# Optimization experiments

Hardware: AMD Instinct MI355X
Metric: run time of the kernel (lower is better)

Reference implementation:

```python
import jax, jax.numpy as jnp
import numpy as np

SEQ, BS, IN, H, NUM_LAYERS = 512, 64, 1024, 1024, 2


def setup_inputs() -> dict:
    key = jax.random.key(0)
    k1, k2, k3, k4 = jax.random.split(key, 4)

    def xavier(k, shape):
        fan_in, fan_out = shape
        lim = jnp.sqrt(6.0 / (fan_in + fan_out))
        return jax.random.uniform(k, shape, jnp.float32, -lim, lim)

    return {
        "x": jax.random.normal(k1, (SEQ, BS, IN), jnp.float32),
        "W_ii0": xavier(k2, (IN, 4 * H)),
        "W_ii": xavier(k3, (H, 4 * H)),
        "W_hi": xavier(k4, (H, 4 * H)),
        "bias": jnp.zeros((4 * H,), jnp.float32),
    }


def _run_layer(x, W_in, W_hi, bias, hidden):
    # x: [seq, bs, feat]; precompute input projection for all timesteps at once
    xw = jnp.einsum('sbf,fg->sbg', x, W_in) + bias  # [seq, bs, 4H]
    bs = x.shape[1]

    def step(carry, xw_t):
        h, c = carry
        gates = xw_t + h @ W_hi  # [bs, 4H]
        i_t = jax.nn.sigmoid(gates[:, :hidden])
        f_t = jax.nn.sigmoid(gates[:, hidden:2 * hidden])
        g_t = jnp.tanh(gates[:, 2 * hidden:3 * hidden])
        o_t = jax.nn.sigmoid(gates[:, 3 * hidden:])
        c = f_t * c + i_t * g_t
        h = o_t * jnp.tanh(c)
        return (h, c), h

    h0 = jnp.zeros((bs, hidden), x.dtype)
    c0 = jnp.zeros((bs, hidden), x.dtype)
    (h, c), hs = jax.lax.scan(step, (h0, c0), xw)
    return hs, h, c  # hs: [seq, bs, hidden]


def reference(x, W_ii0, W_ii, W_hi, bias):
    h = c = None
    for l in range(NUM_LAYERS):
        W_in = W_ii0 if l == 0 else W_ii
        x, h, c = _run_layer(x, W_in, W_hi, bias, H)
    return x, (h, c)
```

## Files before the change

### kernel.cpp

```cpp
#include <hip/hip_runtime.h>

typedef __attribute__((ext_vector_type(8))) short short8;
typedef __attribute__((ext_vector_type(4))) float floatx4;

#define SEQ 512
#define BS  64
#define HID 1024
#define G4  4096
#define NBLK 128
#define NGRP 4
#define BPG  32
#define GBS  16
#define UPB  32

__device__ __forceinline__ unsigned short f2b(float f) {
  union { float f; unsigned u; } v; v.f = f;
  return (unsigned short)((v.u + 0x7FFFu + ((v.u >> 16) & 1u)) >> 16);
}
__device__ __forceinline__ float b2f(unsigned short s) {
  union { unsigned u; float f; } v; v.u = ((unsigned)s) << 16;
  return v.f;
}

__device__ __forceinline__ void gload_lds16_cc(const void* g, void* l) {
  __builtin_amdgcn_global_load_lds(
      (const __attribute__((address_space(1))) unsigned int*)g,
      (__attribute__((address_space(3))) unsigned int*)l,
      16, 0, 17);
}

__global__ void wtrans(const float* __restrict__ W, short* __restrict__ WT) {
  __shared__ float tile[32][33];
  const int tx = threadIdx.x, ty = threadIdx.y;
  const int n0 = blockIdx.x << 5, k0 = blockIdx.y << 5;
#pragma unroll
  for (int i = 0; i < 32; i += 8)
    tile[ty + i][tx] = W[(size_t)(k0 + ty + i) * G4 + n0 + tx];
  __syncthreads();
#pragma unroll
  for (int i = 0; i < 32; i += 8)
    WT[(size_t)(n0 + ty + i) * 1024 + k0 + tx] = (short)f2b(tile[tx][ty + i]);
}

__global__ __launch_bounds__(256)
void conv_bf16(const float* __restrict__ in, unsigned short* __restrict__ out) {
  const size_t i = ((size_t)blockIdx.x * 256 + threadIdx.x) * 8;
  const floatx4 a = *(const floatx4*)(in + i);
  const floatx4 b = *(const floatx4*)(in + i + 4);
  short8 s;
#pragma unroll
  for (int e = 0; e < 4; ++e) { s[e] = (short)f2b(a[e]); s[4 + e] = (short)f2b(b[e]); }
  *(short8*)(out + i) = s;
}

struct FusedArgs {
  const unsigned short* xw;
  const short* wt_hi;
  unsigned short* hbuf;
  float* cbuf;
  unsigned int* cnt;
  float* hs;
  unsigned short* hsb;
  float* h_final;
  float* c_final;
  int t0, t1, wr_final;
  const short* A;
  const short* BT;
  const float* bias;
  unsigned short* dst;
  int Mrows, genable;
};

__device__ __forceinline__ void scan_body(const FusedArgs& p, char* smem) {
  const int tid = threadIdx.x;
  const int wave = tid >> 6, lane = tid & 63;
  const int lr = lane & 15, lh = lane >> 4;
  const int blk = blockIdx.x;
  const int g = blk >> 5;
  const int ub_idx = blk & 31;
  const int u_new = (wave << 2) + (lr >> 2);
  const int gcol = ((lr & 3) << 10) + ub_idx * UPB + u_new;

  short8 breg[32];
  {
    const short* wp = p.wt_hi + (size_t)gcol * HID + (lh << 3);
#pragma unroll
    for (int kk = 0; kk < 32; ++kk) breg[kk] = *(const short8*)(wp + (kk << 5));
  }

  const int b_new = (lh << 2) + (lr & 3);
  const int ci = ((g * GBS + b_new) << 10) + ub_idx * UPB + u_new;
  float creg = p.cbuf[ci];
  const int asw = lr & 7;
  const int j0 = lr & 1, j1 = (lr >> 1) & 1;

  for (int t = p.t0; t < p.t1; ++t) {
    float xv[4];
#pragma unroll
    for (int r = 0; r < 4; ++r) {
      const size_t rowi = (size_t)(t - p.t0) * BS + g * GBS + (lh << 2) + r;
      xv[r] = b2f(p.xw[rowi * G4 + gcol]);
    }

    if (t > 0 && wave == 0) {
      const unsigned long long cad =
          (unsigned long long)(p.cnt + ((size_t)t * NGRP + g) * 16);
      unsigned f0;
      for (;;) {
        asm volatile("global_load_dword %0, %1, off sc0 sc1\n\t"
                     "s_waitcnt vmcnt(0)"
                     : "=v"(f0) : "v"(cad) : "memory");
        if (f0 >= BPG) break;
        __builtin_amdgcn_s_sleep(1);
      }
    }
    __syncthreads();

    const unsigned short* hb = p.hbuf + (size_t)(t & 1) * (BS * HID) + (size_t)g * GBS * HID;
    unsigned short* hw = p.hbuf + (size_t)((t + 1) & 1) * (BS * HID) + (size_t)g * GBS * HID;

    {
      const int spans[4] = { 2 * wave, 2 * wave + 16, 2 * wave + 1, 2 * wave + 17 };
#pragma unroll
      for (int j = 0; j < 4; ++j) {
        const int i = spans[j];
        const int row = i >> 1, half = i & 1;
        const int chunk = ((half << 6) + lane) ^ (row & 7);
        gload_lds16_cc(hb + row * HID + (chunk << 3), smem + (i << 10));
      }
    }
    asm volatile("s_waitcnt vmcnt(2)" ::: "memory");
    __builtin_amdgcn_s_barrier();
    __builtin_amdgcn_sched_barrier(0);

    floatx4 acc = {0.f, 0.f, 0.f, 0.f};
#pragma unroll
    for (int kk = 0; kk < 16; ++kk) {
      const int kc = (kk << 2) + lh;
      const short8 afr = *(const short8*)(smem + (lr << 11) + ((kc ^ asw) << 4));
      acc = __builtin_amdgcn_mfma_f32_16x16x32_bf16(afr, breg[kk], acc, 0, 0, 0);
    }
    asm volatile("s_waitcnt vmcnt(0)" ::: "memory");
    __builtin_amdgcn_s_barrier();
    __builtin_amdgcn_sched_barrier(0);
#pragma unroll
    for (int kk = 16; kk < 32; ++kk) {
      const int kc = (kk << 2) + lh;
      const short8 afr = *(const short8*)(smem + (lr << 11) + ((kc ^ asw) << 4));
      acc = __builtin_amdgcn_mfma_f32_16x16x32_bf16(afr, breg[kk], acc, 0, 0, 0);
    }

    const float x0 = acc[0] + xv[0], x1 = acc[1] + xv[1];
    const float x2 = acc[2] + xv[2], x3 = acc[3] + xv[3];
    const float s0 = __shfl_xor(x1, 1), s1 = __shfl_xor(x0, 1);
    const float s2 = __shfl_xor(x3, 1), s3 = __shfl_xor(x2, 1);
    const float y0 = j0 ? s0 : x0, y1 = j0 ? x1 : s1;
    const float y2 = j0 ? s2 : x2, y3 = j0 ? x3 : s3;
    const float z0s = __shfl_xor(y2, 2), z1s = __shfl_xor(y3, 2);
    const float z2s = __shfl_xor(y0, 2), z3s = __shfl_xor(y1, 2);
    const float ig = j1 ? z0s : y0;
    const float fg = j1 ? z1s : y1;
    const float gg = j1 ? y2 : z2s;
    const float og = j1 ? y3 : z3s;

    const float iv = 1.f / (1.f + __expf(-ig));
    const float fv = 1.f / (1.f + __expf(-fg));
    const float gv = tanhf(gg);
    const float ov = 1.f / (1.f + __expf(-og));
    const float cn = fv * creg + iv * gv;
    creg = cn;
    const float hv = ov * tanhf(cn);
    const unsigned hv16 = (unsigned)f2b(hv);

    {
      const unsigned other = (unsigned)__shfl_xor((int)hv16, 4, 64);
      if ((lr & 4) == 0) {
        const unsigned val = (hv16 & 0xFFFFu) | (other << 16);
        const unsigned long long dst =
            (unsigned long long)(hw + (size_t)b_new * HID + ub_idx * UPB + u_new);
        asm volatile("global_store_dword %0, %1, off sc0 sc1"
                     :: "v"(dst), "v"(val) : "memory");
      }
    }
    asm volatile("s_waitcnt vmcnt(0)" ::: "memory");
    __syncthreads();
    if (tid == 0)
      atomicAdd(p.cnt + ((size_t)(t + 1) * NGRP + g) * 16, 1u);

    {
      const size_t oidx = ((size_t)t * BS + g * GBS + b_new) * HID + ub_idx * UPB + u_new;
      p.hs[oidx] = hv;
      p.hsb[oidx] = (unsigned short)hv16;
      if (p.wr_final && t == SEQ - 1) { p.h_final[ci] = hv; p.c_final[ci] = cn; }
    }
  }
  p.cbuf[ci] = creg;
}

__device__ __forceinline__ void gemm_body(const FusedArgs& p, char* smem,
                                          int bi, int gstride) {
  if (!p.genable) return;
  short* Al = (short*)smem;
  short* Bl = (short*)(smem + 10240);
  const int tid = threadIdx.x;
  const int wave = tid >> 6, lane = tid & 63;
  const int lr = lane & 15, lh = lane >> 4;
  const int wm = wave >> 1, wn = wave & 1;
  const int nmt = p.Mrows >> 7;
  const int tot = nmt << 5;
  const int srow = tid >> 2, scol = (tid & 3) << 3;

  for (int tt = bi; tt < tot; tt += gstride) {
    const int m0 = (tt >> 5) << 7, n0 = (tt & 31) << 7;
    const short* aptr = p.A + (size_t)(m0 + srow) * 1024 + scol;
    const short* bptr = p.BT + (size_t)(n0 + srow) * 1024 + scol;
    floatx4 acc[2][4] = {};
    short8 pa = *(const short8*)aptr;
    short8 pb = *(const short8*)bptr;
    for (int it = 0; it < 32; ++it) {
      __syncthreads();
      *(short8*)&Al[srow * 40 + scol] = pa;
      *(short8*)&Bl[srow * 40 + scol] = pb;
      __syncthreads();
      if (it < 31) {
        pa = *(const short8*)(aptr + ((it + 1) << 5));
        pb = *(const short8*)(bptr + ((it + 1) << 5));
      }
      short8 af[2], bf[4];
#pragma unroll
      for (int mt = 0; mt < 2; ++mt)
        af[mt] = *(const short8*)&Al[(wm * 32 + mt * 16 + lr) * 40 + lh * 8];
#pragma unroll
      for (int nt = 0; nt < 4; ++nt)
        bf[nt] = *(const short8*)&Bl[(wn * 64 + nt * 16 + lr) * 40 + lh * 8];
#pragma unroll
      for (int mt = 0; mt < 2; ++mt)
#pragma unroll
        for (int nt = 0; nt < 4; ++nt)
          acc[mt][nt] = __builtin_amdgcn_mfma_f32_16x16x32_bf16(af[mt], bf[nt], acc[mt][nt], 0, 0, 0);
    }
#pragma unroll
    for (int nt = 0; nt < 4; ++nt) {
      const int gc = n0 + wn * 64 + nt * 16 + lr;
      const float bv = p.bias[gc];
#pragma unroll
      for (int mt = 0; mt < 2; ++mt)
#pragma unroll
        for (int r = 0; r < 4; ++r) {
          const int gr = m0 + wm * 32 + mt * 16 + (lh << 2) + r;
          p.dst[(size_t)gr * G4 + gc] = f2b(acc[mt][nt][r] + bv);
        }
    }
  }
}

__global__ __launch_bounds__(512, 2)
void gemm_pre(FusedArgs p) {
  __shared__ __align__(16) char smem[84480];
  gemm_body(p, smem, blockIdx.x, 2 * NBLK);
}

__global__ __launch_bounds__(512, 2)
void lstm_fused(FusedArgs p) {
  __shared__ __align__(16) char smem[84480];
  if (blockIdx.x < NBLK) scan_body(p, smem);
  else                   gemm_body(p, smem, blockIdx.x - NBLK, NBLK);
}

extern "C" void kernel_launch(void* const* d_in, const int* in_sizes, int n_in,
                              void* d_out, int out_size, void* d_ws, size_t ws_size,
                              hipStream_t stream) {
  const float* x    = (const float*)d_in[0];
  const float* Wii0 = (const float*)d_in[1];
  const float* Wii  = (const float*)d_in[2];
  const float* Whi  = (const float*)d_in[3];
  const float* bias = (const float*)d_in[4];
  float* out  = (float*)d_out;
  float* hs   = out;
  float* hfin = out + (size_t)SEQ * BS * HID;
  float* cfin = hfin + BS * HID;

  char* ws = (char*)d_ws;
  short* WT0 = (short*)ws;
  short* WT1 = WT0 + (size_t)G4 * 1024;
  short* WTh = WT1 + (size_t)G4 * 1024;
  unsigned short* hbuf = (unsigned short*)(WTh + (size_t)G4 * 1024);
  float* cbuf = (float*)(hbuf + 2 * BS * HID);
  unsigned int* cnt = (unsigned int*)(cbuf + BS * HID);
  unsigned short* xb = (unsigned short*)(cnt + (size_t)(SEQ + 1) * NGRP * 16);
  char* tail = (char*)(xb + (size_t)SEQ * BS * HID);
  const size_t head = (size_t)(tail - ws);
  const size_t avail = (ws_size > head) ? ws_size - head : 0;
  const size_t perT = (size_t)BS * G4 * 2;

  int chunk;
  if      (avail >= 2 * 128 * perT) chunk = 128;
  else if (avail >= 2 * 64  * perT) chunk = 64;
  else if (avail >= 2 * 32  * perT) chunk = 32;
  else                              chunk = 8;
  const size_t chunkBytes = (size_t)chunk * perT;
  unsigned short* xwbuf[2] = { (unsigned short*)tail,
                               (unsigned short*)(tail + chunkBytes) };
  const int nc = SEQ / chunk;

  wtrans<<<dim3(128, 32), dim3(32, 8), 0, stream>>>(Wii0, WT0);
  wtrans<<<dim3(128, 32), dim3(32, 8), 0, stream>>>(Wii, WT1);
  wtrans<<<dim3(128, 32), dim3(32, 8), 0, stream>>>(Whi, WTh);
  conv_bf16<<<dim3((SEQ * BS * HID) / (256 * 8)), dim3(256), 0, stream>>>(x, xb);

  for (int layer = 0; layer < 2; ++layer) {
    hipMemsetAsync(hbuf, 0, 2 * BS * HID * sizeof(unsigned short), stream);
    hipMemsetAsync(cbuf, 0, BS * HID * sizeof(float), stream);
    hipMemsetAsync(cnt, 0, (size_t)(SEQ + 1) * NGRP * 16 * sizeof(unsigned), stream);

    if (layer == 0) {
      FusedArgs pa = {};
      pa.A = (const short*)xb;
      pa.BT = WT0;
      pa.bias = bias;
      pa.dst = xwbuf[0];
      pa.Mrows = chunk * BS;
      pa.genable = 1;
      gemm_pre<<<dim3(2 * NBLK), dim3(512), 0, stream>>>(pa);
    }

    for (int c = 0; c < nc; ++c) {
      FusedArgs fa;
      fa.xw = xwbuf[c & 1];
      fa.wt_hi = WTh;
      fa.hbuf = hbuf;
      fa.cbuf = cbuf;
      fa.cnt = cnt;
      fa.hs = hs;
      fa.hsb = xb;
      fa.h_final = layer ? hfin : nullptr;
      fa.c_final = layer ? cfin : nullptr;
      fa.t0 = c * chunk;
      fa.t1 = (c + 1) * chunk;
      fa.wr_final = layer;
      fa.bias = bias;
      fa.dst = xwbuf[(c + 1) & 1];
      fa.Mrows = chunk * BS;
      const int nxt = ((c + 1) % nc) * chunk * BS;
      fa.A = (const short*)(xb + (size_t)nxt * HID);
      fa.BT = (layer == 0 && c < nc - 1) ? WT0 : WT1;
      fa.genable = !(layer == 1 && c == nc - 1);
      void* args[] = { &fa };
      hipLaunchCooperativeKernel(reinterpret_cast<const void*>(&lstm_fused),
                                 dim3(2 * NBLK), dim3(512), args, 0u, stream);
    }
  }
}
```

Measured before the change: 4.473 ms.

## Replace per-step atomic counter with per-block flags and stage h outputs through LDS

Cross-block step synchronization moves from one atomic counter per group and step to one flag per block holding the completed timestep. Waiters poll 32 flags in parallel across a wave and wait until all of them reach the step. The hidden-state results are also staged in LDS so that the h exchange buffer, the bf16 copy and the fp32 output are written with wide coalesced stores by separate waves, instead of scattered per-lane stores. The cost is an extra __syncthreads per step, and only wave 0's exchange store plus its flag store sits on the critical path before the next step's wait.

```diff
diff --git a/kernel.cpp b/kernel.cpp
--- a/kernel.cpp
+++ b/kernel.cpp
@@ -58,7 +58,7 @@
   const short* wt_hi;
   unsigned short* hbuf;
   float* cbuf;
-  unsigned int* cnt;
+  unsigned int* flags;
   float* hs;
   unsigned short* hsb;
   float* h_final;
@@ -72,6 +72,8 @@
 };
 
 __device__ __forceinline__ void scan_body(const FusedArgs& p, char* smem) {
+  unsigned short* hpk = (unsigned short*)(smem + 32768);
+  float* hpf = (float*)(smem + 34048);
   const int tid = threadIdx.x;
   const int wave = tid >> 6, lane = tid & 63;
   const int lr = lane & 15, lh = lane >> 4;
@@ -94,6 +96,9 @@
   const int asw = lr & 7;
   const int j0 = lr & 1, j1 = (lr >> 1) & 1;
 
+  const unsigned long long fad =
+      (unsigned long long)(p.flags + ((size_t)(g * BPG) + (lane & 31)) * 16);
+
   for (int t = p.t0; t < p.t1; ++t) {
     float xv[4];
 #pragma unroll
@@ -103,14 +108,12 @@
     }
 
     if (t > 0 && wave == 0) {
-      const unsigned long long cad =
-          (unsigned long long)(p.cnt + ((size_t)t * NGRP + g) * 16);
       unsigned f0;
       for (;;) {
         asm volatile("global_load_dword %0, %1, off sc0 sc1\n\t"
                      "s_waitcnt vmcnt(0)"
-                     : "=v"(f0) : "v"(cad) : "memory");
-        if (f0 >= BPG) break;
+                     : "=v"(f0) : "v"(fad) : "memory");
+        if (__all(f0 >= (unsigned)t)) break;
         __builtin_amdgcn_s_sleep(1);
       }
     }
@@ -170,28 +173,38 @@
     const float cn = fv * creg + iv * gv;
     creg = cn;
     const float hv = ov * tanhf(cn);
-    const unsigned hv16 = (unsigned)f2b(hv);
-
-    {
-      const unsigned other = (unsigned)__shfl_xor((int)hv16, 4, 64);
-      if ((lr & 4) == 0) {
-        const unsigned val = (hv16 & 0xFFFFu) | (other << 16);
-        const unsigned long long dst =
-            (unsigned long long)(hw + (size_t)b_new * HID + ub_idx * UPB + u_new);
+    const unsigned short hv16 = f2b(hv);
+
+    hpk[b_new * 40 + u_new] = hv16;
+    hpf[b_new * 36 + u_new] = hv;
+    if (p.wr_final && t == SEQ - 1) { p.h_final[ci] = hv; p.c_final[ci] = cn; }
+    __syncthreads();
+
+    if (wave == 0) {
+      const int row = lane >> 2, k = lane & 3;
+      const short8 v = *(const short8*)(smem + 32768 + row * 80 + k * 16);
+      const unsigned long long dst = (unsigned long long)
+          (hw + (size_t)row * HID + ub_idx * UPB + (k << 3));
+      asm volatile("global_store_dwordx4 %0, %1, off sc0 sc1"
+                   :: "v"(dst), "v"(v) : "memory");
+      asm volatile("s_waitcnt vmcnt(0)" ::: "memory");
+      if (lane == 0) {
+        const unsigned long long fdst =
+            (unsigned long long)(p.flags + (size_t)blk * 16);
+        const unsigned fval = (unsigned)(t + 1);
         asm volatile("global_store_dword %0, %1, off sc0 sc1"
-                     :: "v"(dst), "v"(val) : "memory");
+                     :: "v"(fdst), "v"(fval) : "memory");
       }
-    }
-    asm volatile("s_waitcnt vmcnt(0)" ::: "memory");
-    __syncthreads();
-    if (tid == 0)
-      atomicAdd(p.cnt + ((size_t)(t + 1) * NGRP + g) * 16, 1u);
-
-    {
-      const size_t oidx = ((size_t)t * BS + g * GBS + b_new) * HID + ub_idx * UPB + u_new;
-      p.hs[oidx] = hv;
-      p.hsb[oidx] = (unsigned short)hv16;
-      if (p.wr_final && t == SEQ - 1) { p.h_final[ci] = hv; p.c_final[ci] = cn; }
+    } else if (wave == 1) {
+      const int row = lane >> 2, k = lane & 3;
+      const short8 v = *(const short8*)(smem + 32768 + row * 80 + k * 16);
+      *(short8*)(p.hsb + ((size_t)t * BS + g * GBS + row) * HID
+                 + ub_idx * UPB + (k << 3)) = v;
+    } else if (wave < 4) {
+      const int row = ((wave - 2) << 3) + (lane >> 3), k = lane & 7;
+      const floatx4 v = *(const floatx4*)(smem + 34048 + row * 144 + k * 16);
+      *(floatx4*)(p.hs + ((size_t)t * BS + g * GBS + row) * HID
+                  + ub_idx * UPB + (k << 2)) = v;
     }
   }
   p.cbuf[ci] = creg;
@@ -286,8 +299,8 @@
   short* WTh = WT1 + (size_t)G4 * 1024;
   unsigned short* hbuf = (unsigned short*)(WTh + (size_t)G4 * 1024);
   float* cbuf = (float*)(hbuf + 2 * BS * HID);
-  unsigned int* cnt = (unsigned int*)(cbuf + BS * HID);
-  unsigned short* xb = (unsigned short*)(cnt + (size_t)(SEQ + 1) * NGRP * 16);
+  unsigned int* flags = (unsigned int*)(cbuf + BS * HID);
+  unsigned short* xb = (unsigned short*)(flags + NBLK * 16);
   char* tail = (char*)(xb + (size_t)SEQ * BS * HID);
   const size_t head = (size_t)(tail - ws);
   const size_t avail = (ws_size > head) ? ws_size - head : 0;
@@ -311,7 +324,7 @@
   for (int layer = 0; layer < 2; ++layer) {
     hipMemsetAsync(hbuf, 0, 2 * BS * HID * sizeof(unsigned short), stream);
     hipMemsetAsync(cbuf, 0, BS * HID * sizeof(float), stream);
-    hipMemsetAsync(cnt, 0, (size_t)(SEQ + 1) * NGRP * 16 * sizeof(unsigned), stream);
+    hipMemsetAsync(flags, 0, NBLK * 16 * sizeof(unsigned int), stream);
 
     if (layer == 0) {
       FusedArgs pa = {};
@@ -330,7 +343,7 @@
       fa.wt_hi = WTh;
       fa.hbuf = hbuf;
       fa.cbuf = cbuf;
-      fa.cnt = cnt;
+      fa.flags = flags;
       fa.hs = hs;
       fa.hsb = xb;
       fa.h_final = layer ? hfin : nullptr;
```

New measurement: 3.904 ms. 1.15x faster.
